# Performance work log

Measured on AMD Instinct MI355X. Metric: run time of the kernel, lower is better.

The kernel has to match this reference:

```python
import jax, jax.numpy as jnp
import numpy as np

B, S, S2 = 4, 4096, 2048
D, SCAF_D, H = 1024, 768, 8
HD = D // H
BLEND = 0.5
SIG_HALF = 0.6224593312018546  # sigmoid(0.5), initial sparsity_factor
K = max(1, min(S, int(S * SIG_HALF)))  # 2549, static top-k size


def setup_inputs() -> dict:
    key = jax.random.key(0)
    ks = jax.random.split(key, 12)
    s = 0.02
    return {
        "base_hidden": jax.random.normal(ks[0], (B, S, D), jnp.float32),
        "scaffold_hidden": jax.random.normal(ks[1], (B, S2, SCAF_D), jnp.float32),
        "scaffold_proj_w": jax.random.normal(ks[2], (D, SCAF_D), jnp.float32) * s,
        "scaffold_proj_b": jnp.zeros((D,), jnp.float32),
        "topk_w": jax.random.normal(ks[3], (1, D), jnp.float32) * s,
        "topk_b": jnp.zeros((1,), jnp.float32),
        "in_proj_w": jax.random.normal(ks[4], (3 * D, D), jnp.float32) * s,
        "in_proj_b": jnp.zeros((3 * D,), jnp.float32),
        "out_proj_w": jax.random.normal(ks[5], (D, D), jnp.float32) * s,
        "out_proj_b": jnp.zeros((D,), jnp.float32),
        "gate_w": jax.random.normal(ks[6], (1, D), jnp.float32) * s,
        "gate_b": jnp.zeros((1,), jnp.float32),
        "confidence_threshold": jnp.array([0.65], jnp.float32),
    }


def reference(base_hidden, scaffold_hidden, scaffold_proj_w, scaffold_proj_b,
              topk_w, topk_b, in_proj_w, in_proj_b, out_proj_w, out_proj_b,
              gate_w, gate_b, confidence_threshold):
    # scaffold projection: [B,S2,SCAF_D] -> [B,S2,D]
    scaf = jnp.einsum('bsk,dk->bsd', scaffold_hidden, scaffold_proj_w) + scaffold_proj_b
    conf = jnp.mean(jnp.linalg.norm(scaf, axis=-1))

    # learned top-k token selection on base tokens
    scores = jnp.einsum('bsd,od->bso', base_hidden, topk_w)[..., 0] + topk_b[0]  # [B,S]
    _, idx = jax.lax.top_k(scores, K)  # [B,K]
    sparse = jnp.take_along_axis(base_hidden, idx[:, :, None], axis=1)  # [B,K,D]

    # multihead cross-attention: query=sparse tokens, key/value=scaffold
    wq, wk, wv = in_proj_w[:D], in_proj_w[D:2 * D], in_proj_w[2 * D:]
    bq, bk, bv = in_proj_b[:D], in_proj_b[D:2 * D], in_proj_b[2 * D:]
    q = (jnp.einsum('bkd,ed->bke', sparse, wq) + bq).reshape(B, K, H, HD)
    k = (jnp.einsum('bsd,ed->bse', scaf, wk) + bk).reshape(B, S2, H, HD)
    v = (jnp.einsum('bsd,ed->bse', scaf, wv) + bv).reshape(B, S2, H, HD)
    att = jnp.einsum('bqhd,bkhd->bhqk', q, k) / jnp.sqrt(jnp.float32(HD))
    p = jax.nn.softmax(att, axis=-1)
    o = jnp.einsum('bhqk,bkhd->bqhd', p, v).reshape(B, K, D)
    attn_out = jnp.einsum('bkd,ed->bke', o, out_proj_w) + out_proj_b  # [B,K,D]

    # scatter attended tokens back into the full sequence
    b_idx = jnp.arange(B)[:, None]
    attn_full = base_hidden.at[b_idx, idx].set(attn_out)  # [B,S,D]

    gate = jax.nn.sigmoid(jnp.einsum('bsd,od->bso', base_hidden, gate_w) + gate_b)  # [B,S,1]
    augmented = base_hidden + gate * attn_full
    fused = (1.0 - BLEND) * base_hidden + BLEND * augmented
    return jnp.where(conf > confidence_threshold[0], fused, base_hidden)
```

## Files before the change

kernel.cpp:

```cpp
#include <hip/hip_runtime.h>
#include <hip/hip_bf16.h>

typedef unsigned short u16;
typedef unsigned int   u32;
typedef __bf16 bf16x8 __attribute__((ext_vector_type(8)));
typedef float  f32x4  __attribute__((ext_vector_type(4)));

#define B_     4
#define S_     4096
#define S2_    2048
#define D_     1024
#define SCAFD_ 768
#define H_     8
#define HD_    128
#define KSEL_  2549
#define MROWS_ (B_ * KSEL_)
#define QK_SCALE 0.08838834764831845f
#define QBLKS_ ((KSEL_ + 127) / 128)
#define ANWG_  (QBLKS_ * H_ * B_)

#define CN0_ (D_ * SCAFD_ / 4)
#define CN1_ (3 * D_ * D_ / 4)
#define CN2_ (D_ * D_ / 4)

__device__ __forceinline__ float b2f(u16 u){
  union { u32 i; float f; } c; c.i = ((u32)u) << 16; return c.f;
}
__device__ __forceinline__ u16 f2b(float f){
  u32 x = __float_as_uint(f);
  u32 r = x + 0x7fffu + ((x >> 16) & 1u);
  return (u16)(r >> 16);
}
__device__ __forceinline__ u32 pk2(float lo, float hi){
  return (u32)f2b(lo) | ((u32)f2b(hi) << 16);
}
__device__ __forceinline__ f32x4 mfma16(bf16x8 a, bf16x8 b, f32x4 c){
  return __builtin_amdgcn_mfma_f32_16x16x32_bf16(a, b, c, 0, 0, 0);
}
__device__ __forceinline__ void gl_lds16(const u16* g, u16* l){
  __builtin_amdgcn_global_load_lds((const __attribute__((address_space(1))) void*)g,
                                   (__attribute__((address_space(3))) void*)l, 16, 0, 0);
}

__global__ void CrossAttentionFuser_65798898975031_kernel() {}

__global__ __launch_bounds__(256) void cast3_k(
    const float* __restrict__ s0, u16* __restrict__ d0,
    const float* __restrict__ s1, u16* __restrict__ d1,
    const float* __restrict__ s2, u16* __restrict__ d2)
{
  int i = blockIdx.x * 256 + threadIdx.x;
  const float* s; u16* d; int j = i;
  if (j < CN0_){ s = s0; d = d0; }
  else if (j < CN0_ + CN1_){ j -= CN0_; s = s1; d = d1; }
  else { j -= CN0_ + CN1_; s = s2; d = d2; }
  float4 v = ((const float4*)s)[j];
  uint2 o; o.x = pk2(v.x, v.y); o.y = pk2(v.z, v.w);
  ((uint2*)d)[j] = o;
}

__global__ __launch_bounds__(256) void scores_gate_k(
    const float* __restrict__ base, const float* __restrict__ tw, const float* __restrict__ tb,
    const float* __restrict__ gw, const float* __restrict__ gb,
    float* __restrict__ scores, float* __restrict__ gate, float* __restrict__ conf_sum)
{
  int t = threadIdx.x, wave = t >> 6, lane = t & 63;
  if (blockIdx.x == 0 && t == 0) conf_sum[0] = 0.f;
  int row = blockIdx.x * 4 + wave;
  const float* bp  = base + (size_t)row * D_ + lane * 16;
  const float* twp = tw + lane * 16;
  const float* gwp = gw + lane * 16;
  float sd = 0.f, gd = 0.f;
  #pragma unroll
  for (int c = 0; c < 4; c++){
    float4 b4 = *(const float4*)(bp  + c * 4);
    float4 t4 = *(const float4*)(twp + c * 4);
    float4 g4 = *(const float4*)(gwp + c * 4);
    sd = fmaf(b4.x, t4.x, sd); sd = fmaf(b4.y, t4.y, sd);
    sd = fmaf(b4.z, t4.z, sd); sd = fmaf(b4.w, t4.w, sd);
    gd = fmaf(b4.x, g4.x, gd); gd = fmaf(b4.y, g4.y, gd);
    gd = fmaf(b4.z, g4.z, gd); gd = fmaf(b4.w, g4.w, gd);
  }
  #pragma unroll
  for (int off = 32; off > 0; off >>= 1){
    sd += __shfl_xor(sd, off);
    gd += __shfl_xor(gd, off);
  }
  if (lane == 0){
    scores[row] = sd + tb[0];
    gate[row]   = 1.f / (1.f + __expf(-(gd + gb[0])));
  }
}

__global__ __launch_bounds__(1024) void topk_sel_k(
    const float* __restrict__ scores, int* __restrict__ sel_rows, int* __restrict__ sel_pos)
{
  __shared__ unsigned long long keys[4096];
  __shared__ int hist[256];
  __shared__ int wsum[16], woff[16];
  __shared__ int sh_found, sh_Kr;
  int b = blockIdx.x, t = threadIdx.x;
  for (int i = t; i < 4096; i += 1024){
    float s = scores[b * 4096 + i];
    u32 bits = __float_as_uint(s);
    bits = (bits & 0x80000000u) ? ~bits : (bits | 0x80000000u);
    keys[i] = ((unsigned long long)bits << 12) | (unsigned long long)(4095 - i);
  }
  __syncthreads();
  int Kr = KSEL_;
  unsigned long long prefix = 0;
  int shift_prev = 44;
  const int shifts[6] = {36, 28, 20, 12, 4, 0};
  for (int lev = 0; lev < 6; lev++){
    int shift = shifts[lev];
    if (t < 256) hist[t] = 0;
    __syncthreads();
    for (int i = t; i < 4096; i += 1024){
      unsigned long long k = keys[i];
      if ((k >> shift_prev) == prefix)
        atomicAdd(&hist[(int)((k >> shift) & 255)], 1);
    }
    __syncthreads();
    if (t == 0){
      int cum = 0, fb = 0;
      for (int bk = 255; bk >= 0; bk--){
        int h = hist[bk];
        if (cum + h >= Kr){ fb = bk; break; }
        cum += h;
      }
      sh_found = fb; sh_Kr = Kr - cum;
    }
    __syncthreads();
    int gap = shift_prev - shift;
    prefix = (prefix << gap) | (unsigned long long)(sh_found & ((1 << gap) - 1));
    Kr = sh_Kr;
    shift_prev = shift;
    __syncthreads();
  }
  unsigned long long T = prefix;
  int base_i = t * 4;
  int cnt = 0, flags = 0;
  #pragma unroll
  for (int j = 0; j < 4; j++){
    if (keys[base_i + j] >= T){ cnt++; flags |= 1 << j; }
  }
  int lane = t & 63, wv = t >> 6;
  int sc = cnt;
  #pragma unroll
  for (int off = 1; off < 64; off <<= 1){
    int v = __shfl_up(sc, off);
    if (lane >= off) sc += v;
  }
  if (lane == 63) wsum[wv] = sc;
  __syncthreads();
  if (t < 16){
    int acc = 0;
    for (int j = 0; j < 16; j++){ if (j < t) acc += wsum[j]; }
    woff[t] = acc;
  }
  __syncthreads();
  int pos = sc - cnt + woff[wv];
  #pragma unroll
  for (int j = 0; j < 4; j++){
    int s = base_i + j;
    int p = -1;
    if ((flags >> j) & 1){
      p = pos++;
      sel_rows[b * KSEL_ + p] = b * S_ + s;
    }
    sel_pos[b * S_ + s] = p;
  }
}

__global__ __launch_bounds__(256) void gemm128(
    const void* __restrict__ Aptr, int aMode,
    const u16* __restrict__ Wb, const float* __restrict__ bias,
    void* __restrict__ Cptr, int outMode, float outScale,
    const int* __restrict__ rowidx, int M, int N, int Kd)
{
  __shared__ __align__(16) u16 At[128 * 32];
  __shared__ __align__(16) u16 Wt[128 * 32];
  int m0 = blockIdx.x * 128, n0 = blockIdx.y * 128;
  int t = threadIdx.x;
  int lane = t & 63, quad = lane >> 4, l15 = lane & 15;
  int wave = t >> 6, wm = wave >> 1, wn = wave & 1;
  int srow = t >> 2, chunk = t & 3;
  const float* apf[2];
  const u16*   apb[2];
  const u16*   wpp[2];
  #pragma unroll
  for (int r = 0; r < 2; r++){
    int rr = m0 + r * 64 + srow; if (rr > M - 1) rr = M - 1;
    int gr = rowidx ? rowidx[rr] : rr;
    apf[r] = (const float*)Aptr + (size_t)gr * Kd + chunk * 8;
    apb[r] = (const u16*)Aptr   + (size_t)gr * Kd + chunk * 8;
    wpp[r] = Wb + (size_t)(n0 + r * 64 + srow) * Kd + chunk * 8;
  }
  f32x4 acc[4][4];
  #pragma unroll
  for (int mi = 0; mi < 4; mi++){
    #pragma unroll
    for (int ni = 0; ni < 4; ni++){
      f32x4 z = {0.f, 0.f, 0.f, 0.f};
      acc[mi][ni] = z;
    }
  }
  for (int k0 = 0; k0 < Kd; k0 += 32){
    __syncthreads();
    #pragma unroll
    for (int r = 0; r < 2; r++){
      gl_lds16(wpp[r] + k0, Wt + r * 2048 + t * 8);
    }
    if (aMode == 0){
      #pragma unroll
      for (int r = 0; r < 2; r++){
        gl_lds16(apb[r] + k0, At + r * 2048 + t * 8);
      }
    } else {
      #pragma unroll
      for (int r = 0; r < 2; r++){
        float4 a0 = *(const float4*)(apf[r] + k0);
        float4 a1 = *(const float4*)(apf[r] + k0 + 4);
        uint4 av;
        av.x = pk2(a0.x, a0.y); av.y = pk2(a0.z, a0.w);
        av.z = pk2(a1.x, a1.y); av.w = pk2(a1.z, a1.w);
        *(uint4*)(At + r * 2048 + t * 8) = av;
      }
    }
    __syncthreads();
    bf16x8 afr[4], bfr[4];
    #pragma unroll
    for (int mi = 0; mi < 4; mi++){
      afr[mi] = *(const bf16x8*)(At + (wm * 64 + mi * 16 + l15) * 32 + quad * 8);
    }
    #pragma unroll
    for (int ni = 0; ni < 4; ni++){
      bfr[ni] = *(const bf16x8*)(Wt + (wn * 64 + ni * 16 + l15) * 32 + quad * 8);
    }
    #pragma unroll
    for (int mi = 0; mi < 4; mi++){
      #pragma unroll
      for (int ni = 0; ni < 4; ni++){
        acc[mi][ni] = mfma16(afr[mi], bfr[ni], acc[mi][ni]);
      }
    }
  }
  #pragma unroll
  for (int ni = 0; ni < 4; ni++){
    int col = n0 + wn * 64 + ni * 16 + l15;
    float bs = bias[col];
    #pragma unroll
    for (int mi = 0; mi < 4; mi++){
      #pragma unroll
      for (int r = 0; r < 4; r++){
        int row = m0 + wm * 64 + mi * 16 + quad * 4 + r;
        if (row < M){
          float val = (acc[mi][ni][r] + bs) * outScale;
          if (outMode == 0){
            ((u16*)Cptr)[(size_t)row * N + col] = f2b(val);
          } else if (outMode == 1){
            int bb = row >> 11, s2 = row & 2047;
            int hh = col >> 7,  hd = col & 127;
            ((u16*)Cptr)[((size_t)((bb * 8 + hh) * 128 + hd) << 11) + s2] = f2b(val);
          } else {
            ((float*)Cptr)[(size_t)row * N + col] = val;
          }
        }
      }
    }
  }
}

__global__ __launch_bounds__(256) void conf_k(const u16* __restrict__ scaf, float* __restrict__ conf_sum){
  int t = threadIdx.x, wave = t >> 6, lane = t & 63;
  float acc = 0.f;
  for (int i = 0; i < 32; i++){
    int row = blockIdx.x * 128 + wave * 32 + i;
    const u16* rp = scaf + (size_t)row * D_ + lane * 16;
    uint4 v0 = *(const uint4*)rp, v1 = *(const uint4*)(rp + 8);
    float ss = 0.f;
    u32 w[8];
    w[0]=v0.x; w[1]=v0.y; w[2]=v0.z; w[3]=v0.w;
    w[4]=v1.x; w[5]=v1.y; w[6]=v1.z; w[7]=v1.w;
    #pragma unroll
    for (int j = 0; j < 8; j++){
      float lo = b2f(w[j] & 0xffff), hi = b2f(w[j] >> 16);
      ss = fmaf(lo, lo, ss);
      ss = fmaf(hi, hi, ss);
    }
    #pragma unroll
    for (int off = 32; off > 0; off >>= 1){
      ss += __shfl_xor(ss, off);
    }
    if (lane == 0) acc += sqrtf(ss);
  }
  if (lane == 0) atomicAdd(conf_sum, acc);
}

__global__ __launch_bounds__(256) void attn_k(
    const u16* __restrict__ Q, const u16* __restrict__ Kb,
    const u16* __restrict__ Vt, u16* __restrict__ O, int KS)
{
  __shared__ __align__(16) u16 Klds[64][136];
  __shared__ __align__(16) u16 Vtlds[128][72];
  int o = blockIdx.x;
  int id = (o & 7) * (ANWG_ >> 3) + (o >> 3);
  int qblk = id % QBLKS_;
  int rest = id / QBLKS_;
  int h = rest & 7, b = rest >> 3;
  int t = threadIdx.x, wave = t >> 6, lane = t & 63, quad = lane >> 4, l15 = lane & 15;
  int qbase = qblk * 128 + wave * 32;

  bf16x8 aq[2][4];
  #pragma unroll
  for (int ti = 0; ti < 2; ti++){
    int qr = qbase + ti * 16 + l15; if (qr > KS - 1) qr = KS - 1;
    const u16* qp = Q + (size_t)(b * KS + qr) * D_ + h * HD_;
    #pragma unroll
    for (int c = 0; c < 4; c++){
      aq[ti][c] = *(const bf16x8*)(qp + c * 32 + quad * 8);
    }
  }
  float l_i[2];
  f32x4 oa[2][8];
  #pragma unroll
  for (int ti = 0; ti < 2; ti++){
    l_i[ti] = 0.f;
    #pragma unroll
    for (int n = 0; n < 8; n++){
      f32x4 z = {0.f, 0.f, 0.f, 0.f};
      oa[ti][n] = z;
    }
  }
  int krow = t >> 2, kc4 = t & 3;
  int vhd  = t >> 1, vhalf = t & 1;
  const u16* kgp = Kb + (size_t)(b * S2_ + krow) * D_ + h * HD_ + kc4 * 8;
  const u16* vgp = Vt + (size_t)((b * H_ + h) * HD_ + vhd) * S2_ + vhalf * 32;
  int srcA = 32 * (quad & 1) + l15;
  int srcB = srcA + 16;
  bool hiq = (lane & 32) != 0;

  for (int s0 = 0; s0 < S2_; s0 += 64){
    __syncthreads();
    #pragma unroll
    for (int i = 0; i < 4; i++){
      *(uint4*)&Klds[krow][kc4 * 8 + 32 * i]   = *(const uint4*)(kgp + 32 * i);
      *(uint4*)&Vtlds[vhd][vhalf * 32 + 8 * i] = *(const uint4*)(vgp + 8 * i);
    }
    kgp += (size_t)64 * D_;
    vgp += 64;
    __syncthreads();
    #pragma unroll
    for (int ti = 0; ti < 2; ti++){
      f32x4 sc[4];
      #pragma unroll
      for (int tt = 0; tt < 4; tt++){
        f32x4 z = {0.f, 0.f, 0.f, 0.f};
        sc[tt] = z;
      }
      #pragma unroll
      for (int c = 0; c < 4; c++){
        bf16x8 qf = aq[ti][c];
        #pragma unroll
        for (int tt = 0; tt < 4; tt++){
          bf16x8 kf = *(const bf16x8*)&Klds[tt * 16 + l15][c * 32 + quad * 8];
          sc[tt] = mfma16(kf, qf, sc[tt]);
        }
      }
      float p[4][4];
      float ps = 0.f;
      #pragma unroll
      for (int tt = 0; tt < 4; tt++){
        #pragma unroll
        for (int r = 0; r < 4; r++){
          float e = __expf(sc[tt][r]);
          p[tt][r] = e;
          ps += e;
        }
      }
      ps += __shfl_xor(ps, 16);
      ps += __shfl_xor(ps, 32);
      l_i[ti] += ps;
      u32 pp[4][2];
      #pragma unroll
      for (int tt = 0; tt < 4; tt++){
        pp[tt][0] = pk2(p[tt][0], p[tt][1]);
        pp[tt][1] = pk2(p[tt][2], p[tt][3]);
      }
      #pragma unroll
      for (int g = 0; g < 2; g++){
        u32 a0 = (u32)__shfl((int)pp[2*g][0],   srcA);
        u32 b0 = (u32)__shfl((int)pp[2*g+1][0], srcA);
        u32 a1 = (u32)__shfl((int)pp[2*g][1],   srcA);
        u32 b1 = (u32)__shfl((int)pp[2*g+1][1], srcA);
        u32 a2 = (u32)__shfl((int)pp[2*g][0],   srcB);
        u32 b2 = (u32)__shfl((int)pp[2*g+1][0], srcB);
        u32 a3 = (u32)__shfl((int)pp[2*g][1],   srcB);
        u32 b3 = (u32)__shfl((int)pp[2*g+1][1], srcB);
        union { u32 w[4]; bf16x8 v; } pf;
        pf.w[0] = hiq ? b0 : a0;
        pf.w[1] = hiq ? b1 : a1;
        pf.w[2] = hiq ? b2 : a2;
        pf.w[3] = hiq ? b3 : a3;
        #pragma unroll
        for (int n = 0; n < 8; n++){
          bf16x8 vf = *(const bf16x8*)&Vtlds[n * 16 + l15][g * 32 + quad * 8];
          oa[ti][n] = mfma16(vf, pf.v, oa[ti][n]);
        }
      }
    }
  }
  #pragma unroll
  for (int ti = 0; ti < 2; ti++){
    int qrow = qbase + ti * 16 + l15;
    if (qrow < KS){
      float inv = 1.f / l_i[ti];
      size_t rowoff = (size_t)(b * KS + qrow) * D_ + h * HD_;
      #pragma unroll
      for (int n = 0; n < 8; n++){
        uint2 wv;
        wv.x = pk2(oa[ti][n][0] * inv, oa[ti][n][1] * inv);
        wv.y = pk2(oa[ti][n][2] * inv, oa[ti][n][3] * inv);
        *(uint2*)&O[rowoff + n * 16 + quad * 4] = wv;
      }
    }
  }
}

__global__ __launch_bounds__(256) void final_fuse_k(
    const float* __restrict__ base, const float* __restrict__ gate, const int* __restrict__ sel_pos,
    const float* __restrict__ attnout, const float* __restrict__ conf_sum,
    const float* __restrict__ thr, float* __restrict__ out)
{
  int row = blockIdx.x;
  int d0 = threadIdx.x * 4;
  size_t off = (size_t)row * D_ + d0;
  float4 bv = *(const float4*)(base + off);
  bool conf = (conf_sum[0] * (1.0f / (B_ * S2_))) > thr[0];
  float4 ov;
  if (!conf){
    ov = bv;
  } else {
    float g = gate[row] * 0.5f;
    int p = sel_pos[row];
    if (p >= 0){
      int bb = row >> 12;
      float4 av = *(const float4*)(attnout + (size_t)(bb * KSEL_ + p) * D_ + d0);
      ov.x = fmaf(g, av.x, bv.x);
      ov.y = fmaf(g, av.y, bv.y);
      ov.z = fmaf(g, av.z, bv.z);
      ov.w = fmaf(g, av.w, bv.w);
    } else {
      ov.x = fmaf(g, bv.x, bv.x);
      ov.y = fmaf(g, bv.y, bv.y);
      ov.z = fmaf(g, bv.z, bv.z);
      ov.w = fmaf(g, bv.w, bv.w);
    }
  }
  *(float4*)(out + off) = ov;
}

extern "C" void kernel_launch(void* const* d_in, const int* in_sizes, int n_in,
                              void* d_out, int out_size, void* d_ws, size_t ws_size,
                              hipStream_t stream)
{
  (void)in_sizes; (void)n_in; (void)out_size; (void)ws_size;
  const float* base  = (const float*)d_in[0];
  const float* scafh = (const float*)d_in[1];
  const float* spw   = (const float*)d_in[2];
  const float* spb   = (const float*)d_in[3];
  const float* tw    = (const float*)d_in[4];
  const float* tb    = (const float*)d_in[5];
  const float* ipw   = (const float*)d_in[6];
  const float* ipb   = (const float*)d_in[7];
  const float* opw   = (const float*)d_in[8];
  const float* opb   = (const float*)d_in[9];
  const float* gw    = (const float*)d_in[10];
  const float* gb    = (const float*)d_in[11];
  const float* thr   = (const float*)d_in[12];
  float* out = (float*)d_out;

  char* ws = (char*)d_ws;
  size_t off = 0;
  auto alloc = [&](size_t bytes) -> void* {
    void* p = ws + off; off += (bytes + 255) & ~(size_t)255; return p;
  };
  float* conf_sum = (float*)alloc(4);
  float* scores   = (float*)alloc((size_t)B_ * S_ * 4);
  float* gate     = (float*)alloc((size_t)B_ * S_ * 4);
  int*   sel_rows = (int*)alloc((size_t)MROWS_ * 4);
  int*   sel_pos  = (int*)alloc((size_t)B_ * S_ * 4);
  u16*   spwb     = (u16*)alloc((size_t)D_ * SCAFD_ * 2);
  u16*   ipwb     = (u16*)alloc((size_t)3 * D_ * D_ * 2);
  u16*   opwb     = (u16*)alloc((size_t)D_ * D_ * 2);
  u16*   scaf     = (u16*)alloc((size_t)B_ * S2_ * D_ * 2);
  u16*   kbuf     = (u16*)alloc((size_t)B_ * S2_ * D_ * 2);
  u16*   vt       = (u16*)alloc((size_t)B_ * S2_ * D_ * 2);
  u16*   qbuf     = (u16*)alloc((size_t)MROWS_ * D_ * 2);
  float* attnout  = (float*)scaf;

  cast3_k<<<dim3((CN0_ + CN1_ + CN2_) / 256), 256, 0, stream>>>(
      spw, spwb, ipw, ipwb, opw, opwb);

  scores_gate_k<<<dim3(B_ * S_ / 4), 256, 0, stream>>>(base, tw, tb, gw, gb, scores, gate, conf_sum);
  topk_sel_k<<<dim3(B_), 1024, 0, stream>>>(scores, sel_rows, sel_pos);
  gemm128<<<dim3(B_ * S2_ / 128, D_ / 128), 256, 0, stream>>>(
      scafh, 1, spwb, spb, scaf, 0, 1.f, nullptr, B_ * S2_, D_, SCAFD_);
  conf_k<<<dim3(B_ * S2_ / 128), 256, 0, stream>>>(scaf, conf_sum);
  gemm128<<<dim3(B_ * S2_ / 128, D_ / 128), 256, 0, stream>>>(
      scaf, 0, ipwb + (size_t)D_ * D_, ipb + D_, kbuf, 0, 1.f, nullptr, B_ * S2_, D_, D_);
  gemm128<<<dim3(B_ * S2_ / 128, D_ / 128), 256, 0, stream>>>(
      scaf, 0, ipwb + (size_t)2 * D_ * D_, ipb + 2 * D_, vt, 1, 1.f, nullptr, B_ * S2_, D_, D_);
  gemm128<<<dim3((MROWS_ + 127) / 128, D_ / 128), 256, 0, stream>>>(
      base, 1, ipwb, ipb, qbuf, 0, QK_SCALE, sel_rows, MROWS_, D_, D_);
  attn_k<<<dim3(ANWG_), 256, 0, stream>>>(qbuf, kbuf, vt, qbuf, KSEL_);
  gemm128<<<dim3((MROWS_ + 127) / 128, D_ / 128), 256, 0, stream>>>(
      qbuf, 0, opwb, opb, attnout, 2, 1.f, nullptr, MROWS_, D_, D_);
  final_fuse_k<<<dim3(B_ * S_), 256, 0, stream>>>(
      base, gate, sel_pos, attnout, conf_sum, thr, out);
}
```

Measured before the change: 665.9 us.

## Swizzle attention LDS tiles and share K/V fragments across both query subtiles

Replaces the padded K and V^T shared-memory tiles with unpadded tiles whose 16-byte chunks are XOR-swizzled by row, so LDS reads should avoid bank conflicts while using less LDS. The loops are restructured so each K and V fragment read from LDS feeds MFMAs for both 16-row query subtiles, halving LDS reads per tile. It also adds a launch-bounds hint for 3 workgroups per CU. Holding both subtiles' scores and probabilities at once raises register pressure, and the occupancy hint may force spills.

```diff
diff --git a/kernel.cpp b/kernel.cpp
--- a/kernel.cpp
+++ b/kernel.cpp
@@ -297,12 +297,12 @@
   if (lane == 0) atomicAdd(conf_sum, acc);
 }
 
-__global__ __launch_bounds__(256) void attn_k(
+__global__ __launch_bounds__(256, 3) void attn_k(
     const u16* __restrict__ Q, const u16* __restrict__ Kb,
     const u16* __restrict__ Vt, u16* __restrict__ O, int KS)
 {
-  __shared__ __align__(16) u16 Klds[64][136];
-  __shared__ __align__(16) u16 Vtlds[128][72];
+  __shared__ __align__(16) u16 Klds[64 * 128];
+  __shared__ __align__(16) u16 Vtlds[128 * 64];
   int o = blockIdx.x;
   int id = (o & 7) * (ANWG_ >> 3) + (o >> 3);
   int qblk = id % QBLKS_;
@@ -310,6 +310,7 @@
   int h = rest & 7, b = rest >> 3;
   int t = threadIdx.x, wave = t >> 6, lane = t & 63, quad = lane >> 4, l15 = lane & 15;
   int qbase = qblk * 128 + wave * 32;
+  int e7 = l15 & 7;
 
   bf16x8 aq[2][4];
   #pragma unroll
@@ -334,6 +335,7 @@
   }
   int krow = t >> 2, kc4 = t & 3;
   int vhd  = t >> 1, vhalf = t & 1;
+  int krow7 = krow & 7, vhd7 = vhd & 7;
   const u16* kgp = Kb + (size_t)(b * S2_ + krow) * D_ + h * HD_ + kc4 * 8;
   const u16* vgp = Vt + (size_t)((b * H_ + h) * HD_ + vhd) * S2_ + vhalf * 32;
   int srcA = 32 * (quad & 1) + l15;
@@ -344,69 +346,89 @@
     __syncthreads();
     #pragma unroll
     for (int i = 0; i < 4; i++){
-      *(uint4*)&Klds[krow][kc4 * 8 + 32 * i]   = *(const uint4*)(kgp + 32 * i);
-      *(uint4*)&Vtlds[vhd][vhalf * 32 + 8 * i] = *(const uint4*)(vgp + 8 * i);
+      int kch = (kc4 + 4 * i) ^ krow7;
+      int vch = (vhalf * 4 + i) ^ vhd7;
+      *(uint4*)&Klds[krow * 128 + kch * 8]  = *(const uint4*)(kgp + 32 * i);
+      *(uint4*)&Vtlds[vhd * 64 + vch * 8]   = *(const uint4*)(vgp + 8 * i);
     }
     kgp += (size_t)64 * D_;
     vgp += 64;
     __syncthreads();
+
+    f32x4 sc[2][4];
+    #pragma unroll
+    for (int tt = 0; tt < 4; tt++){
+      f32x4 z = {0.f, 0.f, 0.f, 0.f};
+      sc[0][tt] = z; sc[1][tt] = z;
+    }
+    #pragma unroll
+    for (int c = 0; c < 4; c++){
+      bf16x8 q0 = aq[0][c], q1 = aq[1][c];
+      int kch = (c * 4 + quad) ^ e7;
+      #pragma unroll
+      for (int tt = 0; tt < 4; tt++){
+        bf16x8 kf = *(const bf16x8*)&Klds[(tt * 16 + l15) * 128 + kch * 8];
+        sc[0][tt] = mfma16(kf, q0, sc[0][tt]);
+        sc[1][tt] = mfma16(kf, q1, sc[1][tt]);
+      }
+    }
+
+    u32 pp[2][4][2];
     #pragma unroll
     for (int ti = 0; ti < 2; ti++){
-      f32x4 sc[4];
+      float ps = 0.f;
       #pragma unroll
       for (int tt = 0; tt < 4; tt++){
-        f32x4 z = {0.f, 0.f, 0.f, 0.f};
-        sc[tt] = z;
-      }
-      #pragma unroll
-      for (int c = 0; c < 4; c++){
-        bf16x8 qf = aq[ti][c];
-        #pragma unroll
-        for (int tt = 0; tt < 4; tt++){
-          bf16x8 kf = *(const bf16x8*)&Klds[tt * 16 + l15][c * 32 + quad * 8];
-          sc[tt] = mfma16(kf, qf, sc[tt]);
-        }
-      }
-      float p[4][4];
-      float ps = 0.f;
-      #pragma unroll
-      for (int tt = 0; tt < 4; tt++){
-        #pragma unroll
-        for (int r = 0; r < 4; r++){
-          float e = __expf(sc[tt][r]);
-          p[tt][r] = e;
-          ps += e;
-        }
+        float e0 = __expf(sc[ti][tt][0]);
+        float e1 = __expf(sc[ti][tt][1]);
+        float e2 = __expf(sc[ti][tt][2]);
+        float e3 = __expf(sc[ti][tt][3]);
+        ps += (e0 + e1) + (e2 + e3);
+        pp[ti][tt][0] = pk2(e0, e1);
+        pp[ti][tt][1] = pk2(e2, e3);
       }
       ps += __shfl_xor(ps, 16);
       ps += __shfl_xor(ps, 32);
       l_i[ti] += ps;
-      u32 pp[4][2];
-      #pragma unroll
-      for (int tt = 0; tt < 4; tt++){
-        pp[tt][0] = pk2(p[tt][0], p[tt][1]);
-        pp[tt][1] = pk2(p[tt][2], p[tt][3]);
-      }
-      #pragma unroll
-      for (int g = 0; g < 2; g++){
-        u32 a0 = (u32)__shfl((int)pp[2*g][0],   srcA);
-        u32 b0 = (u32)__shfl((int)pp[2*g+1][0], srcA);
-        u32 a1 = (u32)__shfl((int)pp[2*g][1],   srcA);
-        u32 b1 = (u32)__shfl((int)pp[2*g+1][1], srcA);
-        u32 a2 = (u32)__shfl((int)pp[2*g][0],   srcB);
-        u32 b2 = (u32)__shfl((int)pp[2*g+1][0], srcB);
-        u32 a3 = (u32)__shfl((int)pp[2*g][1],   srcB);
-        u32 b3 = (u32)__shfl((int)pp[2*g+1][1], srcB);
-        union { u32 w[4]; bf16x8 v; } pf;
-        pf.w[0] = hiq ? b0 : a0;
-        pf.w[1] = hiq ? b1 : a1;
-        pf.w[2] = hiq ? b2 : a2;
-        pf.w[3] = hiq ? b3 : a3;
-        #pragma unroll
-        for (int n = 0; n < 8; n++){
-          bf16x8 vf = *(const bf16x8*)&Vtlds[n * 16 + l15][g * 32 + quad * 8];
-          oa[ti][n] = mfma16(vf, pf.v, oa[ti][n]);
-        }
+    }
+
+    #pragma unroll
+    for (int g = 0; g < 2; g++){
+      union { u32 w[4]; bf16x8 v; } pf0, pf1;
+      {
+        u32 a0 = (u32)__shfl((int)pp[0][2*g][0],   srcA);
+        u32 b0 = (u32)__shfl((int)pp[0][2*g+1][0], srcA);
+        u32 a1 = (u32)__shfl((int)pp[0][2*g][1],   srcA);
+        u32 b1 = (u32)__shfl((int)pp[0][2*g+1][1], srcA);
+        u32 a2 = (u32)__shfl((int)pp[0][2*g][0],   srcB);
+        u32 b2 = (u32)__shfl((int)pp[0][2*g+1][0], srcB);
+        u32 a3 = (u32)__shfl((int)pp[0][2*g][1],   srcB);
+        u32 b3 = (u32)__shfl((int)pp[0][2*g+1][1], srcB);
+        pf0.w[0] = hiq ? b0 : a0;
+        pf0.w[1] = hiq ? b1 : a1;
+        pf0.w[2] = hiq ? b2 : a2;
+        pf0.w[3] = hiq ? b3 : a3;
+      }
+      {
+        u32 a0 = (u32)__shfl((int)pp[1][2*g][0],   srcA);
+        u32 b0 = (u32)__shfl((int)pp[1][2*g+1][0], srcA);
+        u32 a1 = (u32)__shfl((int)pp[1][2*g][1],   srcA);
+        u32 b1 = (u32)__shfl((int)pp[1][2*g+1][1], srcA);
+        u32 a2 = (u32)__shfl((int)pp[1][2*g][0],   srcB);
+        u32 b2 = (u32)__shfl((int)pp[1][2*g+1][0], srcB);
+        u32 a3 = (u32)__shfl((int)pp[1][2*g][1],   srcB);
+        u32 b3 = (u32)__shfl((int)pp[1][2*g+1][1], srcB);
+        pf1.w[0] = hiq ? b0 : a0;
+        pf1.w[1] = hiq ? b1 : a1;
+        pf1.w[2] = hiq ? b2 : a2;
+        pf1.w[3] = hiq ? b3 : a3;
+      }
+      int vch = (g * 4 + quad) ^ e7;
+      #pragma unroll
+      for (int n = 0; n < 8; n++){
+        bf16x8 vf = *(const bf16x8*)&Vtlds[(n * 16 + l15) * 64 + vch * 8];
+        oa[0][n] = mfma16(vf, pf0.v, oa[0][n]);
+        oa[1][n] = mfma16(vf, pf1.v, oa[1][n]);
       }
     }
   }
```

Measured after the change: 586.9 us. -11.9%, faster.
